# Performance work log

Measured on AMD Instinct MI355X. Metric: run time of the kernel, lower is better.

The kernel has to match this reference:

```python
import jax, jax.numpy as jnp
import numpy as np

INV_148 = 1.0 / 1.48  # scaling to align grids with flat-top gaussian


def _trilinear_sample(grid, pts):
    # grid: [C, D, H, W]; pts: [N, 3] in (x,y,z)=(W,H,D) normalized coords, align_corners=True,
    # padding_mode='zeros' (out-of-bounds corners contribute 0). Returns [C, N].
    C, D, H, W = grid.shape
    fx = (pts[:, 0] + 1.0) * 0.5 * (W - 1)
    fy = (pts[:, 1] + 1.0) * 0.5 * (H - 1)
    fz = (pts[:, 2] + 1.0) * 0.5 * (D - 1)
    x0 = jnp.floor(fx).astype(jnp.int32)
    y0 = jnp.floor(fy).astype(jnp.int32)
    z0 = jnp.floor(fz).astype(jnp.int32)
    wx, wy, wz = fx - x0, fy - y0, fz - z0
    out = jnp.zeros((C, pts.shape[0]), dtype=grid.dtype)
    for dz in (0, 1):
        for dy in (0, 1):
            for dx in (0, 1):
                xi, yi, zi = x0 + dx, y0 + dy, z0 + dz
                w = (wx if dx else 1.0 - wx) * (wy if dy else 1.0 - wy) * (wz if dz else 1.0 - wz)
                valid = ((xi >= 0) & (xi < W) & (yi >= 0) & (yi < H) & (zi >= 0) & (zi < D))
                v = grid[:, jnp.clip(zi, 0, D - 1), jnp.clip(yi, 0, H - 1), jnp.clip(xi, 0, W - 1)]
                out = out + v * (w * valid)
    return out


def setup_inputs() -> dict:
    key = jax.random.key(0)
    ks = jax.random.split(key, 10)
    G, Fch, Dg, N, NPL, OUT = 32, 2, 64, 524288, 64, 1
    in_dim = G * Fch
    x = jax.random.uniform(ks[0], (N, 3), minval=-1.0, maxval=1.0, dtype=jnp.float32)
    grid_scales = jax.random.uniform(ks[1], (G, 3), minval=1.5, maxval=2.5, dtype=jnp.float32)
    grid_translations = jax.random.uniform(ks[2], (G, 3), minval=-1.0, maxval=1.0, dtype=jnp.float32) * (grid_scales - 1.0)
    feature_grids = jax.random.uniform(ks[3], (G, Fch, Dg, Dg, Dg), minval=-0.001, maxval=0.001, dtype=jnp.float32)
    W0 = jax.random.normal(ks[4], (NPL, in_dim), dtype=jnp.float32) * (1.0 / np.sqrt(in_dim))
    b0 = jnp.zeros((NPL,), dtype=jnp.float32)
    W1 = jax.random.normal(ks[5], (NPL, NPL), dtype=jnp.float32) * (1.0 / np.sqrt(NPL))
    b1 = jnp.zeros((NPL,), dtype=jnp.float32)
    W2 = jax.random.normal(ks[6], (OUT, NPL), dtype=jnp.float32) * (1.0 / np.sqrt(NPL))
    b2 = jnp.zeros((OUT,), dtype=jnp.float32)
    return {"x": x, "grid_scales": grid_scales, "grid_translations": grid_translations,
            "feature_grids": feature_grids, "W0": W0, "b0": b0, "W1": W1, "b1": b1, "W2": W2, "b2": b2}


def reference(x, grid_scales, grid_translations, feature_grids, W0, b0, W1, b1, W2, b2):
    G = feature_grids.shape[0]
    N = x.shape[0]
    # transform(): per-grid affine (diag scale + translation), then * 1/1.48 -> [G, N, 3]
    local = (x[None, :, :] * grid_scales[:, None, :] + grid_translations[:, None, :]) * INV_148
    # forward detaches grid coords before grid_sample
    local = jax.lax.stop_gradient(local)
    feats = jax.vmap(_trilinear_sample)(feature_grids, local)  # [G, F, N]
    h = feats.reshape(G * feats.shape[1], N).T  # [N, G*F]
    h = jax.nn.relu(h @ W0.T + b0)
    h = jax.nn.relu(h @ W1.T + b1)
    return h @ W2.T + b2  # [N, n_outputs]
```

## Files before the change

### kernel.cpp

```cpp
#include <hip/hip_runtime.h>
#include <hip/hip_fp16.h>

#define NG    32
#define DG    64
#define NPL   64
#define CPD2  16
#define NC2   4096
#define NCELL 512
#define HPAD  4
#define BS    512
#define GBS   1024
#define TV    4096
#define HS    68

#define SWZ(i) ((i) ^ (((i) >> 6) & 28))

typedef _Float16 half8 __attribute__((ext_vector_type(8)));
typedef float    floatx4 __attribute__((ext_vector_type(4)));

__global__ void pack_grids_kernel(const float* __restrict__ fg,
                                  uint4* __restrict__ pg, int total4) {
    int idx = blockIdx.x * blockDim.x + threadIdx.x;
    if (idx >= total4) return;
    int g  = idx >> 16;
    int v4 = (idx & 65535) << 2;
    const float* base = fg + ((size_t)g << 19);
    float4 a = *(const float4*)(base + v4);
    float4 b = *(const float4*)(base + (1 << 18) + v4);
    uint4 o;
    __half2 h;
    h = __floats2half2_rn(a.x, b.x); o.x = *(unsigned*)&h;
    h = __floats2half2_rn(a.y, b.y); o.y = *(unsigned*)&h;
    h = __floats2half2_rn(a.z, b.z); o.z = *(unsigned*)&h;
    h = __floats2half2_rn(a.w, b.w); o.w = *(unsigned*)&h;
    pg[idx] = o;
}

__device__ __forceinline__ int morton16(int cx, int cy, int cz) {
    int m = 0;
    #pragma unroll
    for (int b = 0; b < 4; ++b)
        m |= (((cx >> b) & 1) << (3 * b))
           | (((cy >> b) & 1) << (3 * b + 1))
           | (((cz >> b) & 1) << (3 * b + 2));
    return m;
}
__device__ __forceinline__ int cell_of(float px, float py, float pz) {
    int cx = min(max((int)((px + 1.0f) * (0.5f * CPD2)), 0), CPD2 - 1);
    int cy = min(max((int)((py + 1.0f) * (0.5f * CPD2)), 0), CPD2 - 1);
    int cz = min(max((int)((pz + 1.0f) * (0.5f * CPD2)), 0), CPD2 - 1);
    return morton16(cx, cy, cz);
}

__global__ __launch_bounds__(BS)
void hist_kernel(const float* __restrict__ x, int N, int* __restrict__ ghist) {
    __shared__ int lh[NC2];
    for (int i = threadIdx.x; i < NC2; i += BS) lh[i] = 0;
    __syncthreads();
    int n = blockIdx.x * BS + threadIdx.x;
    if (n < N) atomicAdd(&lh[cell_of(x[3*n], x[3*n+1], x[3*n+2])], 1);
    __syncthreads();
    for (int i = threadIdx.x; i < NC2; i += BS) {
        int c = lh[i];
        if (c) atomicAdd(&ghist[i * HPAD], c);
    }
}

__global__ __launch_bounds__(1024)
void scan_kernel(const int* __restrict__ ghist, int* __restrict__ gcursor,
                 int* __restrict__ cellstart) {
    __shared__ int tsum[1024];
    int t = threadIdx.x;
    int v0 = ghist[(t * 4 + 0) * HPAD];
    int v1 = ghist[(t * 4 + 1) * HPAD];
    int v2 = ghist[(t * 4 + 2) * HPAD];
    int v3 = ghist[(t * 4 + 3) * HPAD];
    tsum[t] = v0 + v1 + v2 + v3;
    __syncthreads();
    #pragma unroll
    for (int off = 1; off < 1024; off <<= 1) {
        int u = (t >= off) ? tsum[t - off] : 0;
        __syncthreads();
        tsum[t] += u;
        __syncthreads();
    }
    int base = (t == 0) ? 0 : tsum[t - 1];
    gcursor[(t*4+0)*HPAD] = base; cellstart[t*4+0] = base; base += v0;
    gcursor[(t*4+1)*HPAD] = base; cellstart[t*4+1] = base; base += v1;
    gcursor[(t*4+2)*HPAD] = base; cellstart[t*4+2] = base; base += v2;
    gcursor[(t*4+3)*HPAD] = base; cellstart[t*4+3] = base;
    if (t == 1023) cellstart[NC2] = tsum[1023];
}

__global__ __launch_bounds__(BS)
void scatter_kernel(const float* __restrict__ x, int N,
                    int* __restrict__ gcursor, float4* __restrict__ sorted,
                    int* __restrict__ nidx) {
    __shared__ int cnt[NC2];
    __shared__ int base[NC2];
    int tid = threadIdx.x;
    for (int i = tid; i < NC2; i += BS) cnt[i] = 0;
    __syncthreads();
    int n = blockIdx.x * BS + tid;
    float px = 0.f, py = 0.f, pz = 0.f;
    int c = 0, r = 0;
    bool act = (n < N);
    if (act) {
        px = x[3*n]; py = x[3*n+1]; pz = x[3*n+2];
        c = cell_of(px, py, pz);
        r = atomicAdd(&cnt[c], 1);
    }
    __syncthreads();
    for (int i = tid; i < NC2; i += BS) {
        int cc = cnt[i];
        base[i] = cc ? atomicAdd(&gcursor[i * HPAD], cc) : 0;
    }
    __syncthreads();
    if (act) {
        int pos = base[c] + r;
        sorted[pos] = make_float4(px, py, pz, 0.0f);
        nidx[pos]   = n;
    }
}

__device__ __forceinline__ float2 h2_to_f2(unsigned u) {
    __half2 h = *reinterpret_cast<__half2*>(&u);
    return __half22float2(h);
}

template<bool FAST>
__device__ __forceinline__ unsigned sample_tile(
    const unsigned* __restrict__ tl,
    float px, float py, float pz,
    float A0, float A1, float A2, float B0, float B1, float B2,
    int ox, int oy, int oz)
{
    float fx = fmaf(px, A0, B0);
    float fy = fmaf(py, A1, B1);
    float fz = fmaf(pz, A2, B2);
    float flx = floorf(fx), fly = floorf(fy), flz = floorf(fz);
    int x0 = (int)flx, y0 = (int)fly, z0 = (int)flz;
    float wx = fx - flx, wy = fy - fly, wz = fz - flz;

    float wxa0, wxa1, wya0, wya1, wza0, wza1;
    int ix0, ix1, iy0, iy1, iz0, iz1;
    if (FAST) {
        wxa0 = 1.0f - wx; wxa1 = wx;
        wya0 = 1.0f - wy; wya1 = wy;
        wza0 = 1.0f - wz; wza1 = wz;
        ix0 = x0 - ox;            ix1 = ix0 + 1;
        iy0 = (y0 - oy) << 4;     iy1 = iy0 + 16;
        iz0 = (z0 - oz) << 8;     iz1 = iz0 + 256;
    } else {
        wxa0 = (x0 >= 0  && x0     < DG) ? (1.0f - wx) : 0.0f;
        wxa1 = (x0 >= -1 && x0 + 1 < DG) ? wx          : 0.0f;
        wya0 = (y0 >= 0  && y0     < DG) ? (1.0f - wy) : 0.0f;
        wya1 = (y0 >= -1 && y0 + 1 < DG) ? wy          : 0.0f;
        wza0 = (z0 >= 0  && z0     < DG) ? (1.0f - wz) : 0.0f;
        wza1 = (z0 >= -1 && z0 + 1 < DG) ? wz          : 0.0f;
        ix0 = min(max(x0     - ox, 0), 15);
        ix1 = min(max(x0 + 1 - ox, 0), 15);
        iy0 = (min(max(y0     - oy, 0), 15)) << 4;
        iy1 = (min(max(y0 + 1 - oy, 0), 15)) << 4;
        iz0 = (min(max(z0     - oz, 0), 15)) << 8;
        iz1 = (min(max(z0 + 1 - oz, 0), 15)) << 8;
    }
    const int m0 = (iz0 >> 6) & 28;
    const int m1 = (iz1 >> 6) & 28;

    float w00 = wya0 * wza0, w10 = wya1 * wza0;
    float w01 = wya0 * wza1, w11 = wya1 * wza1;

    float c0 = 0.0f, c1 = 0.0f;
    float2 v;
    v = h2_to_f2(tl[(iz0+iy0+ix0)^m0]); c0 = fmaf(wxa0*w00, v.x, c0); c1 = fmaf(wxa0*w00, v.y, c1);
    v = h2_to_f2(tl[(iz0+iy0+ix1)^m0]); c0 = fmaf(wxa1*w00, v.x, c0); c1 = fmaf(wxa1*w00, v.y, c1);
    v = h2_to_f2(tl[(iz0+iy1+ix0)^m0]); c0 = fmaf(wxa0*w10, v.x, c0); c1 = fmaf(wxa0*w10, v.y, c1);
    v = h2_to_f2(tl[(iz0+iy1+ix1)^m0]); c0 = fmaf(wxa1*w10, v.x, c0); c1 = fmaf(wxa1*w10, v.y, c1);
    v = h2_to_f2(tl[(iz1+iy0+ix0)^m1]); c0 = fmaf(wxa0*w01, v.x, c0); c1 = fmaf(wxa0*w01, v.y, c1);
    v = h2_to_f2(tl[(iz1+iy0+ix1)^m1]); c0 = fmaf(wxa1*w01, v.x, c0); c1 = fmaf(wxa1*w01, v.y, c1);
    v = h2_to_f2(tl[(iz1+iy1+ix0)^m1]); c0 = fmaf(wxa0*w11, v.x, c0); c1 = fmaf(wxa0*w11, v.y, c1);
    v = h2_to_f2(tl[(iz1+iy1+ix1)^m1]); c0 = fmaf(wxa1*w11, v.x, c0); c1 = fmaf(wxa1*w11, v.y, c1);

    __half2 hv = __floats2half2_rn(c0, c1);
    return *reinterpret_cast<unsigned*>(&hv);
}

__global__ __launch_bounds__(GBS)
void gather_kernel(const float4* __restrict__ sorted,
                   const int*   __restrict__ cs16,
                   const float* __restrict__ scales,
                   const float* __restrict__ trans,
                   const unsigned* __restrict__ pg,
                   int4* __restrict__ featbuf, int N)
{
    __shared__ float    sA[NG * 3];
    __shared__ float    sB[NG * 3];
    __shared__ int      sO[NG * 3];
    __shared__ int      sCls[NG];
    __shared__ int      sList[NG + 1];
    __shared__ unsigned tile[2][TV];

    const int tid  = threadIdx.x;
    const int cell = blockIdx.x;
    const int c    = ((cell & 7) << 6) + (cell >> 3);

    int s0c = cs16[c * 8];
    int ec  = cs16[c * 8 + 8];
    if (s0c >= ec) return;

    int cx = (c & 1)        | (((c >> 3) & 1) << 1) | (((c >> 6) & 1) << 2);
    int cy = ((c >> 1) & 1) | (((c >> 4) & 1) << 1) | (((c >> 7) & 1) << 2);
    int cz = ((c >> 2) & 1) | (((c >> 5) & 1) << 1) | (((c >> 8) & 1) << 2);

    if (tid < NG * 3) {
        const float k = (1.0f / 1.48f) * 31.5f;
        float A  = scales[tid] * k;
        float Bv = trans[tid] * k + 31.5f;
        sA[tid] = A; sB[tid] = Bv;
        int d  = tid % 3;
        int cc = (d == 0) ? cx : ((d == 1) ? cy : cz);
        int o  = (int)floorf(fmaf((float)cc * 0.25f - 1.0f, A, Bv));
        sO[tid] = min(max(o, 0), 48);
    }
    __syncthreads();
    if (tid < NG) {
        bool skip = false, fast = true;
        #pragma unroll
        for (int d = 0; d < 3; ++d) {
            float A = sA[3 * tid + d], B = sB[3 * tid + d];
            int  cc = (d == 0) ? cx : ((d == 1) ? cy : cz);
            float lo = fmaf((float)cc, 0.25f, -1.0f) - 1e-4f;
            float hi = lo + 0.25f + 2e-4f;
            float fmn = fmaf(lo, A, B);
            float fmx = fmaf(hi, A, B);
            skip = skip || (fmx <= -1.0f) || (fmn >= 64.0f);
            fast = fast && (fmn >= 0.0f) && (fmx <= 62.9f);
        }
        sCls[tid] = skip ? 0 : (fast ? 1 : 2);
    }
    __syncthreads();
    if (tid == 0) {
        int n2 = 0;
        for (int g = 0; g < NG; ++g)
            if (sCls[g]) sList[n2++] = g;
        sList[NG] = n2;
    }
    __syncthreads();
    const int nAct = sList[NG];

    int  ip0 = s0c + tid,        ip1 = s0c + GBS + tid;
    bool act0 = (ip0 < ec),      act1 = (ip1 < ec);
    float px0 = 0.f, py0 = 0.f, pz0 = 0.f;
    float px1 = 0.f, py1 = 0.f, pz1 = 0.f;
    if (act0) { float4 q = sorted[ip0]; px0 = q.x; py0 = q.y; pz0 = q.z; }
    if (act1) { float4 q = sorted[ip1]; px1 = q.x; py1 = q.y; pz1 = q.z; }

    if (nAct > 0) {
        int g0 = sList[0];
        int ox = sO[3*g0], oy = sO[3*g0+1], oz = sO[3*g0+2];
        const unsigned* gb = pg + ((size_t)g0 << 18);
        #pragma unroll
        for (int jj = 0; jj < 4; ++jj) {
            int v = tid + (jj << 10);
            tile[0][SWZ(v)] = gb[((oz + (v >> 8)) << 12) + ((oy + ((v >> 4) & 15)) << 6)
                                 + ox + (v & 15)];
        }
    }
    __syncthreads();

    unsigned fp0[4], fp1[4];
    unsigned r[4];
    int j = 0;

    #pragma unroll 1
    for (int w = 0; w < 8; ++w) {
        #pragma unroll
        for (int q = 0; q < 4; ++q) {
            int g   = 4 * w + q;
            int cls = sCls[g];
            if (cls == 0) { fp0[q] = 0u; fp1[q] = 0u; continue; }

            const unsigned* tl = &tile[j & 1][0];
            bool more = (j + 1 < nAct);
            if (more) {
                int gn = sList[j + 1];
                int ox = sO[3*gn], oy = sO[3*gn+1], oz = sO[3*gn+2];
                const unsigned* gb = pg + ((size_t)gn << 18);
                #pragma unroll
                for (int jj = 0; jj < 4; ++jj) {
                    int v = tid + (jj << 10);
                    r[jj] = gb[((oz + (v >> 8)) << 12) + ((oy + ((v >> 4) & 15)) << 6)
                               + ox + (v & 15)];
                }
            }

            float A0 = sA[3*g], A1 = sA[3*g+1], A2 = sA[3*g+2];
            float B0 = sB[3*g], B1 = sB[3*g+1], B2 = sB[3*g+2];
            int   ox = sO[3*g], oy = sO[3*g+1], oz = sO[3*g+2];
            fp1[q] = 0u;
            if (cls == 1) {
                fp0[q] = act0 ? sample_tile<true >(tl, px0,py0,pz0, A0,A1,A2,B0,B1,B2, ox,oy,oz) : 0u;
                if (act1)
                    fp1[q] = sample_tile<true >(tl, px1,py1,pz1, A0,A1,A2,B0,B1,B2, ox,oy,oz);
            } else {
                fp0[q] = act0 ? sample_tile<false>(tl, px0,py0,pz0, A0,A1,A2,B0,B1,B2, ox,oy,oz) : 0u;
                if (act1)
                    fp1[q] = sample_tile<false>(tl, px1,py1,pz1, A0,A1,A2,B0,B1,B2, ox,oy,oz);
            }

            if (more) {
                unsigned* td = &tile[(j & 1) ^ 1][0];
                #pragma unroll
                for (int jj = 0; jj < 4; ++jj) {
                    int v = tid + (jj << 10);
                    td[SWZ(v)] = r[jj];
                }
            }
            __syncthreads();
            ++j;
        }
        const size_t plane = (size_t)w * (size_t)N;
        if (act0) featbuf[plane + ip0] =
            make_int4((int)fp0[0], (int)fp0[1], (int)fp0[2], (int)fp0[3]);
        if (act1) featbuf[plane + ip1] =
            make_int4((int)fp1[0], (int)fp1[1], (int)fp1[2], (int)fp1[3]);
    }
}

#define MBS 256
__global__ __launch_bounds__(MBS)
void mlp_kernel(const int4* __restrict__ featbuf,
                const int* __restrict__ nidx,
                const float* __restrict__ W0, const float* __restrict__ b0,
                const float* __restrict__ W1, const float* __restrict__ b1,
                const float* __restrict__ W2, const float* __restrict__ b2,
                float* __restrict__ out, int N)
{
    __shared__ __align__(16) _Float16 sW0h[NPL * NPL];
    __shared__ __align__(16) _Float16 sW1h[NPL * NPL];
    __shared__ float sb0f[NPL], sb1f[NPL], sW2f[NPL];
    __shared__ __align__(16) _Float16 sH[4][NPL * HS];

    int tid = threadIdx.x;
    for (int i = tid; i < NPL * NPL; i += MBS) {
        sW0h[i] = (_Float16)W0[i];
        sW1h[i] = (_Float16)W1[i];
    }
    if (tid < NPL) { sb0f[tid] = b0[tid]; sb1f[tid] = b1[tid]; sW2f[tid] = W2[tid]; }
    __syncthreads();

    const int wave = tid >> 6;
    const int lane = tid & 63;
    const int l15  = lane & 15;
    const int kg   = lane >> 4;
    const long wbase = (long)blockIdx.x * MBS + wave * 64;
    if (wbase >= N) return;

    half8 B0[4][2], B1[4][2];
    float bias0[4], bias1[4], w2v[4];
    #pragma unroll
    for (int nt = 0; nt < 4; ++nt) {
        int ch = nt * 16 + l15;
        #pragma unroll
        for (int kh = 0; kh < 2; ++kh) {
            int k = kh * 32 + kg * 8;
            B0[nt][kh] = *(const half8*)&sW0h[ch * NPL + k];
            B1[nt][kh] = *(const half8*)&sW1h[ch * NPL + k];
        }
        bias0[nt] = sb0f[ch];
        bias1[nt] = sb1f[ch];
        w2v[nt]   = sW2f[ch];
    }

    _Float16* H = &sH[wave][0];

    floatx4 acc[4][4];
    #pragma unroll
    for (int mt = 0; mt < 4; ++mt) {
        long pt = wbase + mt * 16 + l15;
        if (pt > N - 1) pt = N - 1;
        int4 t0 = featbuf[(size_t)kg * N + pt];
        int4 t1 = featbuf[(size_t)(4 + kg) * N + pt];
        half8 a0 = *reinterpret_cast<half8*>(&t0);
        half8 a1 = *reinterpret_cast<half8*>(&t1);
        #pragma unroll
        for (int nt = 0; nt < 4; ++nt) {
            floatx4 cc = {0.f, 0.f, 0.f, 0.f};
            cc = __builtin_amdgcn_mfma_f32_16x16x32_f16(a0, B0[nt][0], cc, 0, 0, 0);
            cc = __builtin_amdgcn_mfma_f32_16x16x32_f16(a1, B0[nt][1], cc, 0, 0, 0);
            acc[mt][nt] = cc;
        }
    }
    #pragma unroll
    for (int mt = 0; mt < 4; ++mt)
        #pragma unroll
        for (int nt = 0; nt < 4; ++nt) {
            int ch = nt * 16 + l15;
            #pragma unroll
            for (int r = 0; r < 4; ++r) {
                float v = fmaxf(acc[mt][nt][r] + bias0[nt], 0.0f);
                H[(mt * 16 + kg * 4 + r) * HS + ch] = (_Float16)v;
            }
        }

    floatx4 acc2[4][4];
    #pragma unroll
    for (int mt = 0; mt < 4; ++mt) {
        const _Float16* hp = &H[(mt * 16 + l15) * HS];
        half8 a0 = *(const half8*)&hp[kg * 8];
        half8 a1 = *(const half8*)&hp[32 + kg * 8];
        #pragma unroll
        for (int nt = 0; nt < 4; ++nt) {
            floatx4 cc = {0.f, 0.f, 0.f, 0.f};
            cc = __builtin_amdgcn_mfma_f32_16x16x32_f16(a0, B1[nt][0], cc, 0, 0, 0);
            cc = __builtin_amdgcn_mfma_f32_16x16x32_f16(a1, B1[nt][1], cc, 0, 0, 0);
            acc2[mt][nt] = cc;
        }
    }

    float p[4][4];
    #pragma unroll
    for (int mt = 0; mt < 4; ++mt)
        #pragma unroll
        for (int r = 0; r < 4; ++r) p[mt][r] = 0.0f;
    #pragma unroll
    for (int mt = 0; mt < 4; ++mt)
        #pragma unroll
        for (int nt = 0; nt < 4; ++nt)
            #pragma unroll
            for (int r = 0; r < 4; ++r) {
                float v = fmaxf(acc2[mt][nt][r] + bias1[nt], 0.0f);
                p[mt][r] = fmaf(v, w2v[nt], p[mt][r]);
            }
    #pragma unroll
    for (int mt = 0; mt < 4; ++mt)
        #pragma unroll
        for (int r = 0; r < 4; ++r) {
            float s = p[mt][r];
            s += __shfl_xor(s, 1);
            s += __shfl_xor(s, 2);
            s += __shfl_xor(s, 4);
            s += __shfl_xor(s, 8);
            p[mt][r] = s;
        }

    float* HF = (float*)H;
    float ob = b2[0];
    if (l15 == 0) {
        #pragma unroll
        for (int mt = 0; mt < 4; ++mt)
            #pragma unroll
            for (int r = 0; r < 4; ++r)
                HF[mt * 16 + kg * 4 + r] = p[mt][r] + ob;
    }
    long pos = wbase + lane;
    if (pos < N) out[nidx[pos]] = HF[lane];
}

__global__ __launch_bounds__(256)
void fused_fallback_kernel(const float* __restrict__ x,
                           const float* __restrict__ scales,
                           const float* __restrict__ trans,
                           const __half2* __restrict__ pg,
                           const float* __restrict__ W0, const float* __restrict__ b0,
                           const float* __restrict__ W1, const float* __restrict__ b1,
                           const float* __restrict__ W2, const float* __restrict__ b2,
                           float* __restrict__ out, int N)
{
    __shared__ float sW0[NPL*NPL], sW1[NPL*NPL], sW2[NPL], sb0[NPL], sb1[NPL];
    __shared__ float sA[NG*3], sB[NG*3];
    const int tid = threadIdx.x;
    for (int i = tid; i < NPL*NPL; i += 256) { sW0[i] = W0[i]; sW1[i] = W1[i]; }
    if (tid < NPL) { sW2[tid] = W2[tid]; sb0[tid] = b0[tid]; sb1[tid] = b1[tid]; }
    if (tid < NG*3) {
        const float k = (1.0f / 1.48f) * 31.5f;
        sA[tid] = scales[tid] * k;
        sB[tid] = trans[tid] * k + 31.5f;
    }
    __syncthreads();
    int n = blockIdx.x * 256 + tid;
    if (n >= N) return;
    float px = x[3*n], py = x[3*n+1], pz = x[3*n+2];
    float feat[2*NG];
    #pragma unroll
    for (int g = 0; g < NG; ++g) {
        float fx = fmaf(px, sA[3*g+0], sB[3*g+0]);
        float fy = fmaf(py, sA[3*g+1], sB[3*g+1]);
        float fz = fmaf(pz, sA[3*g+2], sB[3*g+2]);
        float c0 = 0.f, c1 = 0.f;
        if (fx > -1.f && fx < 64.f && fy > -1.f && fy < 64.f && fz > -1.f && fz < 64.f) {
            float flx = floorf(fx), fly = floorf(fy), flz = floorf(fz);
            int x0 = (int)flx, y0 = (int)fly, z0 = (int)flz;
            float wx = fx-flx, wy = fy-fly, wz = fz-flz;
            float wxa[2], wya[2], wza[2]; int xia[2], yia[2], zia[2];
            wxa[0] = (x0 >= 0  && x0   < DG) ? (1.f-wx) : 0.f;
            wxa[1] = (x0 >= -1 && x0+1 < DG) ? wx : 0.f;
            wya[0] = (y0 >= 0  && y0   < DG) ? (1.f-wy) : 0.f;
            wya[1] = (y0 >= -1 && y0+1 < DG) ? wy : 0.f;
            wza[0] = (z0 >= 0  && z0   < DG) ? (1.f-wz) : 0.f;
            wza[1] = (z0 >= -1 && z0+1 < DG) ? wz : 0.f;
            xia[0] = min(max(x0,0),DG-1); xia[1] = min(max(x0+1,0),DG-1);
            yia[0] = min(max(y0,0),DG-1); yia[1] = min(max(y0+1,0),DG-1);
            zia[0] = min(max(z0,0),DG-1); zia[1] = min(max(z0+1,0),DG-1);
            #pragma unroll
            for (int dz = 0; dz < 2; ++dz)
                #pragma unroll
                for (int dy = 0; dy < 2; ++dy) {
                    int rowoff = (zia[dz] << 12) + (yia[dy] << 6);
                    float wyz = wya[dy] * wza[dz];
                    #pragma unroll
                    for (int dx = 0; dx < 2; ++dx) {
                        float w = wxa[dx] * wyz;
                        float2 vf = __half22float2(pg[(g << 18) + rowoff + xia[dx]]);
                        c0 = fmaf(w, vf.x, c0); c1 = fmaf(w, vf.y, c1);
                    }
                }
        }
        feat[2*g] = c0; feat[2*g+1] = c1;
    }
    float h1[NPL];
    #pragma unroll
    for (int j = 0; j < NPL; j += 2) {
        float a0=0.f,a1=0.f,a2=0.f,a3=0.f;
        const float* r0 = &sW0[j*NPL]; const float* r1 = &sW0[(j+1)*NPL];
        #pragma unroll
        for (int k = 0; k < NPL; k += 2) {
            a0 = fmaf(feat[k],r0[k],a0); a1 = fmaf(feat[k+1],r0[k+1],a1);
            a2 = fmaf(feat[k],r1[k],a2); a3 = fmaf(feat[k+1],r1[k+1],a3);
        }
        h1[j] = fmaxf((a0+a1)+sb0[j],0.f); h1[j+1] = fmaxf((a2+a3)+sb0[j+1],0.f);
    }
    #pragma unroll
    for (int j = 0; j < NPL; j += 2) {
        float a0=0.f,a1=0.f,a2=0.f,a3=0.f;
        const float* r0 = &sW1[j*NPL]; const float* r1 = &sW1[(j+1)*NPL];
        #pragma unroll
        for (int k = 0; k < NPL; k += 2) {
            a0 = fmaf(h1[k],r0[k],a0); a1 = fmaf(h1[k+1],r0[k+1],a1);
            a2 = fmaf(h1[k],r1[k],a2); a3 = fmaf(h1[k+1],r1[k+1],a3);
        }
        feat[j] = fmaxf((a0+a1)+sb1[j],0.f); feat[j+1] = fmaxf((a2+a3)+sb1[j+1],0.f);
    }
    float a0 = 0.f, a1 = 0.f;
    #pragma unroll
    for (int k = 0; k < NPL; k += 2) { a0 = fmaf(feat[k],sW2[k],a0); a1 = fmaf(feat[k+1],sW2[k+1],a1); }
    out[n] = (a0+a1) + b2[0];
}

extern "C" void kernel_launch(void* const* d_in, const int* in_sizes, int n_in,
                              void* d_out, int out_size, void* d_ws, size_t ws_size,
                              hipStream_t stream) {
    const float* x  = (const float*)d_in[0];
    const float* gs = (const float*)d_in[1];
    const float* gt = (const float*)d_in[2];
    const float* fg = (const float*)d_in[3];
    const float* W0 = (const float*)d_in[4];
    const float* b0 = (const float*)d_in[5];
    const float* W1 = (const float*)d_in[6];
    const float* b1 = (const float*)d_in[7];
    const float* W2 = (const float*)d_in[8];
    const float* b2 = (const float*)d_in[9];
    float* out = (float*)d_out;

    const int N = out_size;

    const size_t pg_bytes   = (size_t)NG * (1 << 18) * 4;
    const size_t feat_bytes = (size_t)N * 8 * sizeof(int4);
    const size_t sort_bytes = (size_t)N * sizeof(float4);
    const size_t nidx_bytes = (size_t)N * sizeof(int);
    const size_t cs_bytes   = ((NC2 + 1 + 15) & ~15) * sizeof(int);
    const size_t hist_bytes = (size_t)NC2 * HPAD * sizeof(int);
    const size_t need_full  = pg_bytes + feat_bytes + sort_bytes + nidx_bytes
                            + cs_bytes + 2 * hist_bytes;

    if (ws_size >= need_full) {
        char* w = (char*)d_ws;
        unsigned* pg        = (unsigned*)w;  w += pg_bytes;
        int4*     featbuf   = (int4*)w;      w += feat_bytes;
        float4*   sorted    = (float4*)w;    w += sort_bytes;
        int*      nidx      = (int*)w;       w += nidx_bytes;
        int*      cellstart = (int*)w;       w += cs_bytes;
        int*      ghist     = (int*)w;       w += hist_bytes;
        int*      gcur      = (int*)w;

        int total4 = NG << 16;
        int nblk   = (N + BS - 1) / BS;
        pack_grids_kernel<<<(total4 + 255) / 256, 256, 0, stream>>>(fg, (uint4*)pg, total4);
        hipMemsetAsync(ghist, 0, hist_bytes, stream);
        hist_kernel<<<nblk, BS, 0, stream>>>(x, N, ghist);
        scan_kernel<<<1, 1024, 0, stream>>>(ghist, gcur, cellstart);
        scatter_kernel<<<nblk, BS, 0, stream>>>(x, N, gcur, sorted, nidx);
        gather_kernel<<<NCELL, GBS, 0, stream>>>(
            sorted, cellstart, gs, gt, pg, featbuf, N);
        mlp_kernel<<<(N + MBS - 1) / MBS, MBS, 0, stream>>>(
            featbuf, nidx, W0, b0, W1, b1, W2, b2, out, N);
    } else if (ws_size >= pg_bytes) {
        unsigned* pg = (unsigned*)d_ws;
        int total4 = NG << 16;
        pack_grids_kernel<<<(total4 + 255) / 256, 256, 0, stream>>>(fg, (uint4*)pg, total4);
        fused_fallback_kernel<<<(N + 255) / 256, 256, 0, stream>>>(
            x, gs, gt, (const __half2*)pg, W0, b0, W1, b1, W2, b2, out, N);
    } else {
        fused_fallback_kernel<<<(N + 255) / 256, 256, 0, stream>>>(
            x, gs, gt, (const __half2*)fg, W0, b0, W1, b1, W2, b2, out, N);
    }
}
```

Measured before the change: 186.4 us.

## Split gather into per-(cell,grid) blocks with precomputed active-pair list

Replaces the per-cell gather kernel, which looped over all 32 grids with a double-buffered tile, by one 512-thread block per (cell, grid) pair. A new classify kernel compacts the active pairs to the front of a list so active work is scheduled first. Skipped pairs write zeros. Grid packing and the point histogram are fused into one launch. The feature buffer becomes planar per grid, so the MLP now does eight scalar strided loads per tile instead of two int4 loads, and many more small blocks are launched.

```diff
diff --git a/kernel.cpp b/kernel.cpp
--- a/kernel.cpp
+++ b/kernel.cpp
@@ -7,9 +7,9 @@
 #define CPD2  16
 #define NC2   4096
 #define NCELL 512
-#define HPAD  4
+#define NPAIR (NCELL * NG)
+#define HPAD  16
 #define BS    512
-#define GBS   1024
 #define TV    4096
 #define HS    68
 
@@ -17,24 +17,6 @@
 
 typedef _Float16 half8 __attribute__((ext_vector_type(8)));
 typedef float    floatx4 __attribute__((ext_vector_type(4)));
-
-__global__ void pack_grids_kernel(const float* __restrict__ fg,
-                                  uint4* __restrict__ pg, int total4) {
-    int idx = blockIdx.x * blockDim.x + threadIdx.x;
-    if (idx >= total4) return;
-    int g  = idx >> 16;
-    int v4 = (idx & 65535) << 2;
-    const float* base = fg + ((size_t)g << 19);
-    float4 a = *(const float4*)(base + v4);
-    float4 b = *(const float4*)(base + (1 << 18) + v4);
-    uint4 o;
-    __half2 h;
-    h = __floats2half2_rn(a.x, b.x); o.x = *(unsigned*)&h;
-    h = __floats2half2_rn(a.y, b.y); o.y = *(unsigned*)&h;
-    h = __floats2half2_rn(a.z, b.z); o.z = *(unsigned*)&h;
-    h = __floats2half2_rn(a.w, b.w); o.w = *(unsigned*)&h;
-    pg[idx] = o;
-}
 
 __device__ __forceinline__ int morton16(int cx, int cy, int cz) {
     int m = 0;
@@ -52,17 +34,95 @@
     return morton16(cx, cy, cz);
 }
 
-__global__ __launch_bounds__(BS)
-void hist_kernel(const float* __restrict__ x, int N, int* __restrict__ ghist) {
+__global__ __launch_bounds__(1024)
+void classify_kernel(const float* __restrict__ scales,
+                     const float* __restrict__ trans,
+                     unsigned* __restrict__ pairs, int* __restrict__ counters)
+{
+    __shared__ int   sHead, sTail;
+    __shared__ float sA[NG * 3], sB[NG * 3];
+    const int tid  = threadIdx.x;
+    const int lane = tid & 63;
+    if (tid == 0) { sHead = 0; sTail = NPAIR; }
+    if (tid < NG * 3) {
+        const float k = (1.0f / 1.48f) * 31.5f;
+        sA[tid] = scales[tid] * k;
+        sB[tid] = trans[tid] * k + 31.5f;
+    }
+    __syncthreads();
+
+    for (int p = tid; p < NPAIR; p += 1024) {
+        int c = p >> 5, g = p & 31;
+        int cx = (c & 1)        | (((c >> 3) & 1) << 1) | (((c >> 6) & 1) << 2);
+        int cy = ((c >> 1) & 1) | (((c >> 4) & 1) << 1) | (((c >> 7) & 1) << 2);
+        int cz = ((c >> 2) & 1) | (((c >> 5) & 1) << 1) | (((c >> 8) & 1) << 2);
+        bool skip = false, fast = true;
+        #pragma unroll
+        for (int d = 0; d < 3; ++d) {
+            float A = sA[3 * g + d], B = sB[3 * g + d];
+            int  cc = (d == 0) ? cx : ((d == 1) ? cy : cz);
+            float lo = fmaf((float)cc, 0.25f, -1.0f) - 1e-4f;
+            float hi = lo + 0.25f + 2e-4f;
+            float fmn = fmaf(lo, A, B);
+            float fmx = fmaf(hi, A, B);
+            skip = skip || (fmx <= -1.0f) || (fmn >= 64.0f);
+            fast = fast && (fmn >= 0.0f) && (fmx <= 62.9f);
+        }
+        unsigned code = ((unsigned)c << 6) | ((unsigned)g << 1) | (fast ? 1u : 0u);
+
+        unsigned long long mAct = __ballot(!skip);
+        int cntA = __popcll(mAct);
+        int bA = 0, bS = 0;
+        if (lane == 0) {
+            bA = atomicAdd(&sHead, cntA);
+            bS = atomicAdd(&sTail, -(64 - cntA));
+        }
+        bA = __shfl(bA, 0); bS = __shfl(bS, 0);
+        unsigned long long below = (1ull << lane) - 1ull;
+        if (!skip) pairs[bA + __popcll(mAct & below)] = code;
+        else       pairs[bS - 1 - __popcll(~mAct & below)] = code;
+    }
+    __syncthreads();
+    if (tid == 0) counters[0] = sHead;
+}
+
+__global__ __launch_bounds__(256)
+void pack_hist_kernel(const float* __restrict__ fg, uint4* __restrict__ pg,
+                      int total4, int nPack,
+                      const float* __restrict__ x, int N,
+                      int* __restrict__ ghist)
+{
     __shared__ int lh[NC2];
-    for (int i = threadIdx.x; i < NC2; i += BS) lh[i] = 0;
-    __syncthreads();
-    int n = blockIdx.x * BS + threadIdx.x;
-    if (n < N) atomicAdd(&lh[cell_of(x[3*n], x[3*n+1], x[3*n+2])], 1);
-    __syncthreads();
-    for (int i = threadIdx.x; i < NC2; i += BS) {
-        int c = lh[i];
-        if (c) atomicAdd(&ghist[i * HPAD], c);
+    if ((int)blockIdx.x < nPack) {
+        int idx = blockIdx.x * 256 + threadIdx.x;
+        if (idx >= total4) return;
+        int g  = idx >> 16;
+        int v4 = (idx & 65535) << 2;
+        const float* base = fg + ((size_t)g << 19);
+        float4 a = *(const float4*)(base + v4);
+        float4 b = *(const float4*)(base + (1 << 18) + v4);
+        uint4 o;
+        __half2 h;
+        h = __floats2half2_rn(a.x, b.x); o.x = *(unsigned*)&h;
+        h = __floats2half2_rn(a.y, b.y); o.y = *(unsigned*)&h;
+        h = __floats2half2_rn(a.z, b.z); o.z = *(unsigned*)&h;
+        h = __floats2half2_rn(a.w, b.w); o.w = *(unsigned*)&h;
+        pg[idx] = o;
+    } else {
+        int b = blockIdx.x - nPack;
+        for (int i = threadIdx.x; i < NC2; i += 256) lh[i] = 0;
+        __syncthreads();
+        int base = b * 1024 + threadIdx.x;
+        #pragma unroll
+        for (int s = 0; s < 4; ++s) {
+            int n = base + s * 256;
+            if (n < N) atomicAdd(&lh[cell_of(x[3*n], x[3*n+1], x[3*n+2])], 1);
+        }
+        __syncthreads();
+        for (int i = threadIdx.x; i < NC2; i += 256) {
+            int c = lh[i];
+            if (c) atomicAdd(&ghist[i * HPAD], c);
+        }
     }
 }
 
@@ -186,151 +246,77 @@
     return *reinterpret_cast<unsigned*>(&hv);
 }
 
-__global__ __launch_bounds__(GBS)
-void gather_kernel(const float4* __restrict__ sorted,
-                   const int*   __restrict__ cs16,
-                   const float* __restrict__ scales,
-                   const float* __restrict__ trans,
-                   const unsigned* __restrict__ pg,
-                   int4* __restrict__ featbuf, int N)
+__global__ __launch_bounds__(BS)
+void gather2_kernel(const float4* __restrict__ sorted,
+                    const int*   __restrict__ cs16,
+                    const unsigned* __restrict__ pairs,
+                    const int*   __restrict__ counters,
+                    const float* __restrict__ scales,
+                    const float* __restrict__ trans,
+                    const unsigned* __restrict__ pg,
+                    unsigned* __restrict__ fb, int N)
 {
-    __shared__ float    sA[NG * 3];
-    __shared__ float    sB[NG * 3];
-    __shared__ int      sO[NG * 3];
-    __shared__ int      sCls[NG];
-    __shared__ int      sList[NG + 1];
-    __shared__ unsigned tile[2][TV];
-
-    const int tid  = threadIdx.x;
-    const int cell = blockIdx.x;
-    const int c    = ((cell & 7) << 6) + (cell >> 3);
-
-    int s0c = cs16[c * 8];
-    int ec  = cs16[c * 8 + 8];
-    if (s0c >= ec) return;
+    __shared__ unsigned tile[TV];
+
+    const int tid = threadIdx.x;
+    const int nA  = counters[0];
+    unsigned pr   = pairs[blockIdx.x];
+    const int c   = pr >> 6;
+    const int g   = (pr >> 1) & 31;
+    const bool fastp = pr & 1;
+
+    int s0 = cs16[c * 8];
+    int e  = cs16[c * 8 + 8];
+
+    if ((int)blockIdx.x >= nA) {
+        for (int i = s0 + tid; i < e; i += BS) fb[(size_t)g * N + i] = 0u;
+        return;
+    }
+    if (s0 >= e) return;
 
     int cx = (c & 1)        | (((c >> 3) & 1) << 1) | (((c >> 6) & 1) << 2);
     int cy = ((c >> 1) & 1) | (((c >> 4) & 1) << 1) | (((c >> 7) & 1) << 2);
     int cz = ((c >> 2) & 1) | (((c >> 5) & 1) << 1) | (((c >> 8) & 1) << 2);
 
-    if (tid < NG * 3) {
-        const float k = (1.0f / 1.48f) * 31.5f;
-        float A  = scales[tid] * k;
-        float Bv = trans[tid] * k + 31.5f;
-        sA[tid] = A; sB[tid] = Bv;
-        int d  = tid % 3;
-        int cc = (d == 0) ? cx : ((d == 1) ? cy : cz);
-        int o  = (int)floorf(fmaf((float)cc * 0.25f - 1.0f, A, Bv));
-        sO[tid] = min(max(o, 0), 48);
-    }
-    __syncthreads();
-    if (tid < NG) {
-        bool skip = false, fast = true;
-        #pragma unroll
-        for (int d = 0; d < 3; ++d) {
-            float A = sA[3 * tid + d], B = sB[3 * tid + d];
-            int  cc = (d == 0) ? cx : ((d == 1) ? cy : cz);
-            float lo = fmaf((float)cc, 0.25f, -1.0f) - 1e-4f;
-            float hi = lo + 0.25f + 2e-4f;
-            float fmn = fmaf(lo, A, B);
-            float fmx = fmaf(hi, A, B);
-            skip = skip || (fmx <= -1.0f) || (fmn >= 64.0f);
-            fast = fast && (fmn >= 0.0f) && (fmx <= 62.9f);
-        }
-        sCls[tid] = skip ? 0 : (fast ? 1 : 2);
-    }
-    __syncthreads();
-    if (tid == 0) {
-        int n2 = 0;
-        for (int g = 0; g < NG; ++g)
-            if (sCls[g]) sList[n2++] = g;
-        sList[NG] = n2;
-    }
-    __syncthreads();
-    const int nAct = sList[NG];
-
-    int  ip0 = s0c + tid,        ip1 = s0c + GBS + tid;
-    bool act0 = (ip0 < ec),      act1 = (ip1 < ec);
-    float px0 = 0.f, py0 = 0.f, pz0 = 0.f;
-    float px1 = 0.f, py1 = 0.f, pz1 = 0.f;
-    if (act0) { float4 q = sorted[ip0]; px0 = q.x; py0 = q.y; pz0 = q.z; }
-    if (act1) { float4 q = sorted[ip1]; px1 = q.x; py1 = q.y; pz1 = q.z; }
-
-    if (nAct > 0) {
-        int g0 = sList[0];
-        int ox = sO[3*g0], oy = sO[3*g0+1], oz = sO[3*g0+2];
-        const unsigned* gb = pg + ((size_t)g0 << 18);
-        #pragma unroll
-        for (int jj = 0; jj < 4; ++jj) {
-            int v = tid + (jj << 10);
-            tile[0][SWZ(v)] = gb[((oz + (v >> 8)) << 12) + ((oy + ((v >> 4) & 15)) << 6)
-                                 + ox + (v & 15)];
-        }
-    }
-    __syncthreads();
-
-    unsigned fp0[4], fp1[4];
-    unsigned r[4];
-    int j = 0;
-
-    #pragma unroll 1
-    for (int w = 0; w < 8; ++w) {
-        #pragma unroll
-        for (int q = 0; q < 4; ++q) {
-            int g   = 4 * w + q;
-            int cls = sCls[g];
-            if (cls == 0) { fp0[q] = 0u; fp1[q] = 0u; continue; }
-
-            const unsigned* tl = &tile[j & 1][0];
-            bool more = (j + 1 < nAct);
-            if (more) {
-                int gn = sList[j + 1];
-                int ox = sO[3*gn], oy = sO[3*gn+1], oz = sO[3*gn+2];
-                const unsigned* gb = pg + ((size_t)gn << 18);
-                #pragma unroll
-                for (int jj = 0; jj < 4; ++jj) {
-                    int v = tid + (jj << 10);
-                    r[jj] = gb[((oz + (v >> 8)) << 12) + ((oy + ((v >> 4) & 15)) << 6)
-                               + ox + (v & 15)];
-                }
-            }
-
-            float A0 = sA[3*g], A1 = sA[3*g+1], A2 = sA[3*g+2];
-            float B0 = sB[3*g], B1 = sB[3*g+1], B2 = sB[3*g+2];
-            int   ox = sO[3*g], oy = sO[3*g+1], oz = sO[3*g+2];
-            fp1[q] = 0u;
-            if (cls == 1) {
-                fp0[q] = act0 ? sample_tile<true >(tl, px0,py0,pz0, A0,A1,A2,B0,B1,B2, ox,oy,oz) : 0u;
-                if (act1)
-                    fp1[q] = sample_tile<true >(tl, px1,py1,pz1, A0,A1,A2,B0,B1,B2, ox,oy,oz);
-            } else {
-                fp0[q] = act0 ? sample_tile<false>(tl, px0,py0,pz0, A0,A1,A2,B0,B1,B2, ox,oy,oz) : 0u;
-                if (act1)
-                    fp1[q] = sample_tile<false>(tl, px1,py1,pz1, A0,A1,A2,B0,B1,B2, ox,oy,oz);
-            }
-
-            if (more) {
-                unsigned* td = &tile[(j & 1) ^ 1][0];
-                #pragma unroll
-                for (int jj = 0; jj < 4; ++jj) {
-                    int v = tid + (jj << 10);
-                    td[SWZ(v)] = r[jj];
-                }
-            }
-            __syncthreads();
-            ++j;
-        }
-        const size_t plane = (size_t)w * (size_t)N;
-        if (act0) featbuf[plane + ip0] =
-            make_int4((int)fp0[0], (int)fp0[1], (int)fp0[2], (int)fp0[3]);
-        if (act1) featbuf[plane + ip1] =
-            make_int4((int)fp1[0], (int)fp1[1], (int)fp1[2], (int)fp1[3]);
+    const float k = (1.0f / 1.48f) * 31.5f;
+    float A0 = scales[3*g+0] * k, B0 = trans[3*g+0] * k + 31.5f;
+    float A1 = scales[3*g+1] * k, B1 = trans[3*g+1] * k + 31.5f;
+    float A2 = scales[3*g+2] * k, B2 = trans[3*g+2] * k + 31.5f;
+    int ox = min(max((int)floorf(fmaf((float)cx * 0.25f - 1.0f, A0, B0)), 0), 48);
+    int oy = min(max((int)floorf(fmaf((float)cy * 0.25f - 1.0f, A1, B1)), 0), 48);
+    int oz = min(max((int)floorf(fmaf((float)cz * 0.25f - 1.0f, A2, B2)), 0), 48);
+
+    float4 q0, q1, q2;
+    int  i0 = s0 + tid, i1 = s0 + BS + tid, i2 = s0 + 2 * BS + tid;
+    bool a0_ = (i0 < e), a1_ = (i1 < e), a2_ = (i2 < e);
+    q0 = a0_ ? sorted[i0] : make_float4(0,0,0,0);
+    q1 = a1_ ? sorted[i1] : make_float4(0,0,0,0);
+    q2 = a2_ ? sorted[i2] : make_float4(0,0,0,0);
+
+    const unsigned* gb = pg + ((size_t)g << 18);
+    #pragma unroll
+    for (int jj = 0; jj < 8; ++jj) {
+        int v = tid + (jj << 9);
+        tile[SWZ(v)] = gb[((oz + (v >> 8)) << 12) + ((oy + ((v >> 4) & 15)) << 6)
+                          + ox + (v & 15)];
+    }
+    __syncthreads();
+
+    unsigned* dst = fb + (size_t)g * N;
+    if (fastp) {
+        if (a0_) dst[i0] = sample_tile<true >(tile, q0.x,q0.y,q0.z, A0,A1,A2,B0,B1,B2, ox,oy,oz);
+        if (a1_) dst[i1] = sample_tile<true >(tile, q1.x,q1.y,q1.z, A0,A1,A2,B0,B1,B2, ox,oy,oz);
+        if (a2_) dst[i2] = sample_tile<true >(tile, q2.x,q2.y,q2.z, A0,A1,A2,B0,B1,B2, ox,oy,oz);
+    } else {
+        if (a0_) dst[i0] = sample_tile<false>(tile, q0.x,q0.y,q0.z, A0,A1,A2,B0,B1,B2, ox,oy,oz);
+        if (a1_) dst[i1] = sample_tile<false>(tile, q1.x,q1.y,q1.z, A0,A1,A2,B0,B1,B2, ox,oy,oz);
+        if (a2_) dst[i2] = sample_tile<false>(tile, q2.x,q2.y,q2.z, A0,A1,A2,B0,B1,B2, ox,oy,oz);
     }
 }
 
 #define MBS 256
 __global__ __launch_bounds__(MBS)
-void mlp_kernel(const int4* __restrict__ featbuf,
+void mlp_kernel(const unsigned* __restrict__ fb,
                 const int* __restrict__ nidx,
                 const float* __restrict__ W0, const float* __restrict__ b0,
                 const float* __restrict__ W1, const float* __restrict__ b1,
@@ -357,7 +343,7 @@
     const long wbase = (long)blockIdx.x * MBS + wave * 64;
     if (wbase >= N) return;
 
-    half8 B0[4][2], B1[4][2];
+    half8 B0f[4][2], B1f[4][2];
     float bias0[4], bias1[4], w2v[4];
     #pragma unroll
     for (int nt = 0; nt < 4; ++nt) {
@@ -365,8 +351,8 @@
         #pragma unroll
         for (int kh = 0; kh < 2; ++kh) {
             int k = kh * 32 + kg * 8;
-            B0[nt][kh] = *(const half8*)&sW0h[ch * NPL + k];
-            B1[nt][kh] = *(const half8*)&sW1h[ch * NPL + k];
+            B0f[nt][kh] = *(const half8*)&sW0h[ch * NPL + k];
+            B1f[nt][kh] = *(const half8*)&sW1h[ch * NPL + k];
         }
         bias0[nt] = sb0f[ch];
         bias1[nt] = sb1f[ch];
@@ -380,15 +366,17 @@
     for (int mt = 0; mt < 4; ++mt) {
         long pt = wbase + mt * 16 + l15;
         if (pt > N - 1) pt = N - 1;
-        int4 t0 = featbuf[(size_t)kg * N + pt];
-        int4 t1 = featbuf[(size_t)(4 + kg) * N + pt];
+        const unsigned* p0 = fb + (size_t)(4 * kg) * N + pt;
+        const unsigned* p1 = fb + (size_t)(16 + 4 * kg) * N + pt;
+        uint4 t0 = make_uint4(p0[0], p0[N], p0[2*(size_t)N], p0[3*(size_t)N]);
+        uint4 t1 = make_uint4(p1[0], p1[N], p1[2*(size_t)N], p1[3*(size_t)N]);
         half8 a0 = *reinterpret_cast<half8*>(&t0);
         half8 a1 = *reinterpret_cast<half8*>(&t1);
         #pragma unroll
         for (int nt = 0; nt < 4; ++nt) {
             floatx4 cc = {0.f, 0.f, 0.f, 0.f};
-            cc = __builtin_amdgcn_mfma_f32_16x16x32_f16(a0, B0[nt][0], cc, 0, 0, 0);
-            cc = __builtin_amdgcn_mfma_f32_16x16x32_f16(a1, B0[nt][1], cc, 0, 0, 0);
+            cc = __builtin_amdgcn_mfma_f32_16x16x32_f16(a0, B0f[nt][0], cc, 0, 0, 0);
+            cc = __builtin_amdgcn_mfma_f32_16x16x32_f16(a1, B0f[nt][1], cc, 0, 0, 0);
             acc[mt][nt] = cc;
         }
     }
@@ -413,8 +401,8 @@
         #pragma unroll
         for (int nt = 0; nt < 4; ++nt) {
             floatx4 cc = {0.f, 0.f, 0.f, 0.f};
-            cc = __builtin_amdgcn_mfma_f32_16x16x32_f16(a0, B1[nt][0], cc, 0, 0, 0);
-            cc = __builtin_amdgcn_mfma_f32_16x16x32_f16(a1, B1[nt][1], cc, 0, 0, 0);
+            cc = __builtin_amdgcn_mfma_f32_16x16x32_f16(a0, B1f[nt][0], cc, 0, 0, 0);
+            cc = __builtin_amdgcn_mfma_f32_16x16x32_f16(a1, B1f[nt][1], cc, 0, 0, 0);
             acc2[mt][nt] = cc;
         }
     }
@@ -456,6 +444,24 @@
     }
     long pos = wbase + lane;
     if (pos < N) out[nidx[pos]] = HF[lane];
+}
+
+__global__ void pack_only_kernel(const float* __restrict__ fg,
+                                 uint4* __restrict__ pg, int total4) {
+    int idx = blockIdx.x * blockDim.x + threadIdx.x;
+    if (idx >= total4) return;
+    int g  = idx >> 16;
+    int v4 = (idx & 65535) << 2;
+    const float* base = fg + ((size_t)g << 19);
+    float4 a = *(const float4*)(base + v4);
+    float4 b = *(const float4*)(base + (1 << 18) + v4);
+    uint4 o;
+    __half2 h;
+    h = __floats2half2_rn(a.x, b.x); o.x = *(unsigned*)&h;
+    h = __floats2half2_rn(a.y, b.y); o.y = *(unsigned*)&h;
+    h = __floats2half2_rn(a.z, b.z); o.z = *(unsigned*)&h;
+    h = __floats2half2_rn(a.w, b.w); o.w = *(unsigned*)&h;
+    pg[idx] = o;
 }
 
 __global__ __launch_bounds__(256)
@@ -565,40 +571,48 @@
 
     const int N = out_size;
 
-    const size_t pg_bytes   = (size_t)NG * (1 << 18) * 4;
-    const size_t feat_bytes = (size_t)N * 8 * sizeof(int4);
-    const size_t sort_bytes = (size_t)N * sizeof(float4);
-    const size_t nidx_bytes = (size_t)N * sizeof(int);
-    const size_t cs_bytes   = ((NC2 + 1 + 15) & ~15) * sizeof(int);
-    const size_t hist_bytes = (size_t)NC2 * HPAD * sizeof(int);
-    const size_t need_full  = pg_bytes + feat_bytes + sort_bytes + nidx_bytes
-                            + cs_bytes + 2 * hist_bytes;
+    const size_t pg_bytes    = (size_t)NG * (1 << 18) * 4;
+    const size_t fb_bytes    = (size_t)N * NG * 4;
+    const size_t sort_bytes  = (size_t)N * sizeof(float4);
+    const size_t nidx_bytes  = (size_t)N * sizeof(int);
+    const size_t cs_bytes    = ((NC2 + 1 + 15) & ~15) * sizeof(int);
+    const size_t hist_bytes  = (size_t)NC2 * HPAD * sizeof(int);
+    const size_t pairs_bytes = (size_t)NPAIR * 4;
+    const size_t ctr_bytes   = 64;
+    const size_t need_full   = pg_bytes + fb_bytes + sort_bytes + nidx_bytes
+                             + cs_bytes + 2 * hist_bytes + pairs_bytes + ctr_bytes;
 
     if (ws_size >= need_full) {
         char* w = (char*)d_ws;
         unsigned* pg        = (unsigned*)w;  w += pg_bytes;
-        int4*     featbuf   = (int4*)w;      w += feat_bytes;
+        unsigned* fb        = (unsigned*)w;  w += fb_bytes;
         float4*   sorted    = (float4*)w;    w += sort_bytes;
         int*      nidx      = (int*)w;       w += nidx_bytes;
         int*      cellstart = (int*)w;       w += cs_bytes;
         int*      ghist     = (int*)w;       w += hist_bytes;
-        int*      gcur      = (int*)w;
+        int*      gcur      = (int*)w;       w += hist_bytes;
+        unsigned* pairs     = (unsigned*)w;  w += pairs_bytes;
+        int*      counters  = (int*)w;
 
         int total4 = NG << 16;
-        int nblk   = (N + BS - 1) / BS;
-        pack_grids_kernel<<<(total4 + 255) / 256, 256, 0, stream>>>(fg, (uint4*)pg, total4);
+        int nPack  = total4 / 256;
+        int nHist  = (N + 1023) / 1024;
+        int nblkS  = (N + BS - 1) / BS;
+
+        classify_kernel<<<1, 1024, 0, stream>>>(gs, gt, pairs, counters);
         hipMemsetAsync(ghist, 0, hist_bytes, stream);
-        hist_kernel<<<nblk, BS, 0, stream>>>(x, N, ghist);
+        pack_hist_kernel<<<nPack + nHist, 256, 0, stream>>>(
+            fg, (uint4*)pg, total4, nPack, x, N, ghist);
         scan_kernel<<<1, 1024, 0, stream>>>(ghist, gcur, cellstart);
-        scatter_kernel<<<nblk, BS, 0, stream>>>(x, N, gcur, sorted, nidx);
-        gather_kernel<<<NCELL, GBS, 0, stream>>>(
-            sorted, cellstart, gs, gt, pg, featbuf, N);
+        scatter_kernel<<<nblkS, BS, 0, stream>>>(x, N, gcur, sorted, nidx);
+        gather2_kernel<<<NPAIR, BS, 0, stream>>>(
+            sorted, cellstart, pairs, counters, gs, gt, pg, fb, N);
         mlp_kernel<<<(N + MBS - 1) / MBS, MBS, 0, stream>>>(
-            featbuf, nidx, W0, b0, W1, b1, W2, b2, out, N);
+            fb, nidx, W0, b0, W1, b1, W2, b2, out, N);
     } else if (ws_size >= pg_bytes) {
         unsigned* pg = (unsigned*)d_ws;
         int total4 = NG << 16;
-        pack_grids_kernel<<<(total4 + 255) / 256, 256, 0, stream>>>(fg, (uint4*)pg, total4);
+        pack_only_kernel<<<(total4 + 255) / 256, 256, 0, stream>>>(fg, (uint4*)pg, total4);
         fused_fallback_kernel<<<(N + 255) / 256, 256, 0, stream>>>(
             x, gs, gt, (const __half2*)pg, W0, b0, W1, b1, W2, b2, out, N);
     } else {
```

Result: no change. 186.8 us (+0.2%).
